# Optimization experiments

Measured on AMD Instinct MI355X. Metric: run time of the kernel, lower is better.

The kernel has to match this reference:

```python
import jax, jax.numpy as jnp
import numpy as np

RADIUS = 0.1
NSAMPLE = 32
B, N, NPOINT, C = 4, 8192, 2048, 64


def ball_query(xyz, new_xyz, fps_idx):
    """Faithful to pointnet2 ball_query CUDA kernel: for each centroid collect up to
    NSAMPLE in-radius point indices in scan order; slots beyond the count are padded
    with the first in-radius index (0 if the ball is empty). fps_idx is prepended."""
    n = xyz.shape[1]
    # squared distances (B, npoint, N)
    d2 = jnp.sum((new_xyz[:, :, None, :] - xyz[:, None, :, :]) ** 2, axis=-1)
    valid = d2 < jnp.float32(RADIUS) ** 2
    cand = jnp.where(valid, jnp.arange(n, dtype=jnp.int32), jnp.int32(n))
    cand = jnp.sort(cand, axis=-1)[:, :, :NSAMPLE]  # first NSAMPLE valid ids, N = sentinel
    first = cand[:, :, :1]
    pad = jnp.where(first < n, first, 0)            # pad with first valid (0 if none)
    idx = jnp.where(cand < n, cand, pad)
    return jnp.concatenate([fps_idx[:, :, None], idx], axis=2)  # (B, npoint, NSAMPLE+1)


def group(features, idx):
    # features (B, C, N), idx (B, npoint, K) -> (B, C, npoint, K)
    return jax.vmap(lambda f, i: f[:, i])(features, idx)


def setup_inputs() -> dict:
    key = jax.random.key(0)
    k1, k2, k3 = jax.random.split(key, 3)
    xyz = jax.random.uniform(k1, (B, N, 3), dtype=jnp.float32)
    fps_idx = jax.random.randint(k2, (B, NPOINT), 0, N, dtype=jnp.int32)
    new_xyz = jax.vmap(lambda p, i: p[i])(xyz, fps_idx)  # centroids are real points
    features = jax.random.normal(k3, (B, C, N), dtype=jnp.float32)
    return {"xyz": xyz, "new_xyz": new_xyz, "features": features, "fps_idx": fps_idx}


def reference(xyz, new_xyz, features, fps_idx):
    idx = jax.lax.stop_gradient(ball_query(xyz, new_xyz, fps_idx))
    grouped_xyz = group(jnp.swapaxes(xyz, 1, 2), idx)              # (B, 3, npoint, K)
    centered = grouped_xyz - jnp.swapaxes(new_xyz, 1, 2)[..., None]
    # NOTE: the torch module uses in-place `grouped_xyz -= ...`, so raw_grouped_xyz
    # aliases the centered tensor -> both concat slots hold centered coordinates.
    grouped_features = group(features, idx)                        # (B, C, npoint, K)
    return jnp.concatenate([centered, centered, grouped_features], axis=1)
```

## Files before the change

kernel.cpp:

```cpp
#include <hip/hip_runtime.h>
#include <stdint.h>
#include <limits.h>

constexpr int BB      = 4;
constexpr int NN      = 8192;
constexpr int NPOINT  = 2048;
constexpr int CC      = 64;
constexpr int NSAMPLE = 32;
constexpr int KTOT    = NSAMPLE + 1;
constexpr int NCH     = 3 + 3 + CC;
constexpr int CHS     = NPOINT * KTOT;

constexpr int   GG     = 5;
constexpr int   NCELL  = GG * GG * GG;
constexpr float RPADF  = 0.1001f;
constexpr int   CAND_CAP = 192;

__device__ __forceinline__ int cell_of(float x, float y, float z) {
    int ix = (int)floorf(x * 5.0f); ix = ix < 0 ? 0 : (ix > 4 ? 4 : ix);
    int iy = (int)floorf(y * 5.0f); iy = iy < 0 ? 0 : (iy > 4 ? 4 : iy);
    int iz = (int)floorf(z * 5.0f); iz = iz < 0 ? 0 : (iz > 4 ? 4 : iz);
    return (ix * GG + iy) * GG + iz;
}

__global__ __launch_bounds__(1024) void grid_hist_scan(
    const float* __restrict__ xyz, int* __restrict__ cellstartg,
    int* __restrict__ cursorg)
{
    __shared__ int hist[NCELL];
    __shared__ int csl[NCELL + 1];
    const int b = blockIdx.x;
    const int t = threadIdx.x;
    if (t < NCELL) hist[t] = 0;
    __syncthreads();
    const float* xb = xyz + (size_t)b * NN * 3;
#pragma unroll
    for (int k = 0; k < NN / 1024; ++k) {
        const float* p = xb + (size_t)(t + k * 1024) * 3;
        atomicAdd(&hist[cell_of(p[0], p[1], p[2])], 1);
    }
    __syncthreads();
    if (t < 64) {
        int x0 = hist[t];
        int x1 = (t + 64 < NCELL) ? hist[t + 64] : 0;
#pragma unroll
        for (int d = 1; d < 64; d <<= 1) {
            int t0 = __shfl_up(x0, d);
            int t1 = __shfl_up(x1, d);
            if (t >= d) { x0 += t0; x1 += t1; }
        }
        x1 += __shfl(x0, 63);
        if (t == 0) csl[0] = 0;
        csl[1 + t] = x0;
        if (t <= 60) csl[65 + t] = x1;
    }
    __syncthreads();
    if (t < NCELL + 1) cellstartg[b * (NCELL + 1) + t] = csl[t];
    if (t < NCELL)     cursorg[b * NCELL + t]          = csl[t];
}

__global__ __launch_bounds__(256) void scatter_aos(
    const float* __restrict__ xyz, int* __restrict__ cursor,
    float4* __restrict__ spt)
{
    const int t = blockIdx.x * 256 + threadIdx.x;
    if (t >= BB * NN) return;
    const int b = t >> 13;
    const int n = t & (NN - 1);
    const float* p = xyz + (size_t)t * 3;
    const float x = p[0], y = p[1], z = p[2];
    const int c = cell_of(x, y, z);
    const int pos = atomicAdd(&cursor[b * NCELL + c], 1);
    spt[b * NN + pos] = make_float4(x, y, z, __int_as_float(n));
}

__global__ __launch_bounds__(256) void ball_query_grid(
    const float4* __restrict__ spt, const int* __restrict__ cellstart,
    const float* __restrict__ new_xyz, const int* __restrict__ fps_idx,
    int*         __restrict__ idx_out)
{
    __shared__ int cand[4][CAND_CAP];
    const int w    = threadIdx.x >> 6;
    const int lane = threadIdx.x & 63;
    const int wave = blockIdx.x * 4 + w;
    const int b    = wave >> 11;

    const float* cp = new_xyz + (size_t)wave * 3;
    const float cx = cp[0], cy = cp[1], cz = cp[2];
    const float r2 = __fmul_rn(0.1f, 0.1f);

    int ix0 = (int)floorf((cx - RPADF) * 5.0f); ix0 = ix0 < 0 ? 0 : ix0;
    int ix1 = (int)floorf((cx + RPADF) * 5.0f); ix1 = ix1 > 4 ? 4 : ix1;
    int iy0 = (int)floorf((cy - RPADF) * 5.0f); iy0 = iy0 < 0 ? 0 : iy0;
    int iy1 = (int)floorf((cy + RPADF) * 5.0f); iy1 = iy1 > 4 ? 4 : iy1;
    int iz0 = (int)floorf((cz - RPADF) * 5.0f); iz0 = iz0 < 0 ? 0 : iz0;
    int iz1 = (int)floorf((cz + RPADF) * 5.0f); iz1 = iz1 > 4 ? 4 : iz1;

    const int* cs = cellstart + b * (NCELL + 1);
    const int gb  = b * NN;
    int cnt = 0;

    for (int ix = ix0; ix <= ix1; ++ix) {
        for (int iy = iy0; iy <= iy1; ++iy) {
            const int cbase = (ix * GG + iy) * GG;
            const int st = cs[cbase + iz0];
            const int en = cs[cbase + iz1 + 1];
            for (int base = st; base < en; base += 64) {
                const int pos = base + lane;
                const bool inb = pos < en;
                const float4 q = spt[gb + (inb ? pos : st)];
                const int oid = __float_as_int(q.w);
                const float dx = __fsub_rn(cx, q.x);
                const float dy = __fsub_rn(cy, q.y);
                const float dz = __fsub_rn(cz, q.z);
                const float d2 = __fadd_rn(__fadd_rn(__fmul_rn(dx, dx), __fmul_rn(dy, dy)),
                                           __fmul_rn(dz, dz));
                const bool valid = inb && (d2 < r2);
                const unsigned long long m = __ballot(valid);
                if (m != 0ull) {
                    const int prefix = __builtin_amdgcn_mbcnt_hi(
                        (unsigned)(m >> 32), __builtin_amdgcn_mbcnt_lo((unsigned)m, 0u));
                    const int slot = cnt + prefix;
                    if (valid && slot < CAND_CAP) cand[w][slot] = oid;
                    cnt += (int)__popcll(m);
                }
            }
        }
    }

    const int K = cnt > CAND_CAP ? CAND_CAP : cnt;

    int v0 = (lane       < K) ? cand[w][lane]       : INT_MAX;
    int v1 = (lane + 64  < K) ? cand[w][lane + 64]  : INT_MAX;
    int v2 = (lane + 128 < K) ? cand[w][lane + 128] : INT_MAX;
    int rk0 = 0, rk1 = 0, rk2 = 0;
    for (int j = 0; j < K; ++j) {
        const int sv = cand[w][j];
        rk0 += (sv < v0); rk1 += (sv < v1); rk2 += (sv < v2);
    }
    int* out = idx_out + (size_t)wave * KTOT;
    if (lane       < K && rk0 < NSAMPLE) out[1 + rk0] = v0;
    if (lane + 64  < K && rk1 < NSAMPLE) out[1 + rk1] = v1;
    if (lane + 128 < K && rk2 < NSAMPLE) out[1 + rk2] = v2;

    if (K < NSAMPLE) {
        int mn = v0;
#pragma unroll
        for (int off = 32; off >= 1; off >>= 1) {
            const int o = __shfl_xor(mn, off);
            mn = o < mn ? o : mn;
        }
        const int pad = (K > 0) ? mn : 0;
        if (lane >= K && lane < NSAMPLE) out[1 + lane] = pad;
    }
    if (lane == 0) out[0] = fps_idx[wave];
}

__global__ __launch_bounds__(256) void feat_transpose(
    const float* __restrict__ f, float* __restrict__ ft)
{
    __shared__ float tile[64 * 65];
    const int blk = blockIdx.x;
    const int b   = blk >> 7;
    const int n0  = (blk & 127) << 6;
    const int w   = threadIdx.x >> 6, l = threadIdx.x & 63;
#pragma unroll
    for (int i = 0; i < 16; ++i) {
        const int c = i * 4 + w;
        tile[l * 65 + c] = f[((size_t)b * CC + c) * NN + n0 + l];
    }
    __syncthreads();
#pragma unroll
    for (int i = 0; i < 16; ++i) {
        const int flat = i * 256 + threadIdx.x;
        ft[((size_t)b * NN + n0) * CC + flat] = tile[(flat >> 6) * 65 + (flat & 63)];
    }
}

__global__ __launch_bounds__(256) void gather_v4(
    const float* __restrict__ xyz, const float* __restrict__ new_xyz,
    const float4* __restrict__ ft4, const int* __restrict__ idx,
    float* __restrict__ out)
{
    const int gt = blockIdx.x * 256 + threadIdx.x;
    const int o  = gt >> 2;
    const int g  = gt & 3;
    if (o >= BB * CHS) return;
    const int id = idx[o];
    const int b  = o / CHS;
    const int jj = o - b * CHS;
    const size_t outbase = (size_t)b * NCH * CHS + jj;

    if (g < 3) {
        const float pv = xyz[(size_t)(b * NN + id) * 3 + g];
        const float cv = new_xyz[(size_t)(o / KTOT) * 3 + g];
        const float d  = __fsub_rn(pv, cv);
        out[outbase + (size_t)g * CHS]       = d;
        out[outbase + (size_t)(g + 3) * CHS] = d;
    }

    const float4* row = ft4 + ((size_t)b * NN + id) * (CC / 4);
    float4 v[4];
#pragma unroll
    for (int i = 0; i < 4; ++i) v[i] = row[i * 4 + g];
#pragma unroll
    for (int i = 0; i < 4; ++i) {
        const size_t base = outbase + (size_t)(6 + 16 * i + 4 * g) * CHS;
        out[base]           = v[i].x;
        out[base + CHS]     = v[i].y;
        out[base + 2 * CHS] = v[i].z;
        out[base + 3 * CHS] = v[i].w;
    }
}

__global__ __launch_bounds__(256) void ball_query_bf(
    const float* __restrict__ xyz, const float* __restrict__ new_xyz,
    const int* __restrict__ fps_idx, int* __restrict__ idx_out)
{
    const int wave = (blockIdx.x * blockDim.x + threadIdx.x) >> 6;
    const int lane = threadIdx.x & 63;
    if (wave >= BB * NPOINT) return;
    const int b = wave >> 11;
    const float* cp = new_xyz + (size_t)wave * 3;
    const float cx = cp[0], cy = cp[1], cz = cp[2];
    const float r2 = __fmul_rn(0.1f, 0.1f);
    const float* xb = xyz + (size_t)b * NN * 3;
    int* out = idx_out + (size_t)wave * KTOT;
    int count = 0, first = 0;
    for (int base = 0; base < NN; base += 64) {
        const int p = base + lane;
        const float dx = __fsub_rn(cx, xb[p * 3 + 0]);
        const float dy = __fsub_rn(cy, xb[p * 3 + 1]);
        const float dz = __fsub_rn(cz, xb[p * 3 + 2]);
        const float d2 = __fadd_rn(__fadd_rn(__fmul_rn(dx, dx), __fmul_rn(dy, dy)),
                                   __fmul_rn(dz, dz));
        const bool valid = d2 < r2;
        const unsigned long long m = __ballot(valid);
        if (count == 0 && m != 0ull) first = base + __builtin_ctzll(m);
        const int prefix = __builtin_amdgcn_mbcnt_hi(
            (unsigned)(m >> 32), __builtin_amdgcn_mbcnt_lo((unsigned)m, 0u));
        const int slot = count + prefix;
        if (valid && slot < NSAMPLE) out[1 + slot] = p;
        count += (int)__popcll(m);
        if (count >= NSAMPLE) break;
    }
    if (count < NSAMPLE) {
        const int pad = (count > 0) ? first : 0;
        if (lane >= count && lane < NSAMPLE) out[1 + lane] = pad;
    }
    if (lane == 0) out[0] = fps_idx[wave];
}

__global__ __launch_bounds__(256) void gather_kernel(
    const float* __restrict__ xyz, const float* __restrict__ new_xyz,
    const float* __restrict__ features, const int* __restrict__ idx,
    float* __restrict__ out)
{
    const long long total = (long long)BB * NCH * CHS;
    const long long o = (long long)blockIdx.x * blockDim.x + threadIdx.x;
    if (o >= total) return;
    const int s  = (int)(o % KTOT);
    long long t  = o / KTOT;
    const int j  = (int)(t % NPOINT);
    t /= NPOINT;
    const int ch = (int)(t % NCH);
    const int b  = (int)(t / NCH);
    const int id = idx[(long long)(b * NPOINT + j) * KTOT + s];
    float v;
    if (ch < 6) {
        const int c3 = (ch >= 3) ? (ch - 3) : ch;
        v = __fsub_rn(xyz[((long long)b * NN + id) * 3 + c3],
                      new_xyz[((long long)b * NPOINT + j) * 3 + c3]);
    } else {
        v = features[((long long)b * CC + (ch - 6)) * NN + id];
    }
    out[o] = v;
}

extern "C" void kernel_launch(void* const* d_in, const int* in_sizes, int n_in,
                              void* d_out, int out_size, void* d_ws, size_t ws_size,
                              hipStream_t stream) {
    const float* xyz      = (const float*)d_in[0];
    const float* new_xyz  = (const float*)d_in[1];
    const float* features = (const float*)d_in[2];
    const int*   fps_idx  = (const int*)d_in[3];
    float*       out      = (float*)d_out;

    const size_t off_idx  = 0;
    const size_t sz_idx   = (size_t)BB * CHS * 4;
    const size_t off_ft   = off_idx + sz_idx;
    const size_t sz_ft    = (size_t)BB * NN * CC * 4;
    const size_t off_spt  = off_ft + sz_ft;
    const size_t sz_spt   = (size_t)BB * NN * 16;
    const size_t off_cs   = off_spt + sz_spt;
    const size_t sz_cs    = (size_t)BB * (NCELL + 1) * 4;
    const size_t off_cur  = off_cs + 2048;
    const size_t need_full = off_cur + 2048;

    int* idxbuf = (int*)((char*)d_ws + off_idx);
    const int gblocks4 = (BB * CHS * 4 + 255) / 256;

    if (ws_size >= need_full) {
        float*  ft   = (float*) ((char*)d_ws + off_ft);
        float4* spt  = (float4*)((char*)d_ws + off_spt);
        int*    cs   = (int*)   ((char*)d_ws + off_cs);
        int*    cur  = (int*)   ((char*)d_ws + off_cur);

        grid_hist_scan<<<BB, 1024, 0, stream>>>(xyz, cs, cur);
        scatter_aos<<<(BB * NN) / 256, 256, 0, stream>>>(xyz, cur, spt);

        ball_query_grid<<<BB * NPOINT / 4, 256, 0, stream>>>(
            spt, cs, new_xyz, fps_idx, idxbuf);

        feat_transpose<<<BB * (NN / 64), 256, 0, stream>>>(features, ft);
        gather_v4<<<gblocks4, 256, 0, stream>>>(xyz, new_xyz, (const float4*)ft,
                                                idxbuf, out);
    } else if (ws_size >= sz_idx) {
        ball_query_bf<<<BB * NPOINT / 4, 256, 0, stream>>>(xyz, new_xyz, fps_idx, idxbuf);
        const long long total = (long long)BB * NCH * CHS;
        gather_kernel<<<(int)((total + 255) / 256), 256, 0, stream>>>(
            xyz, new_xyz, features, idxbuf, out);
    }
}
```

Measured before the change: 133.9 us.

## Fuse grid histogram with scatter and stage gather output through shared-memory tile

Merges the grid histogram/scan kernel and the scatter kernel into one per-batch kernel that keeps point coordinates and cell ids in registers and uses shared-memory cursors instead of global atomics. This removes one launch and the global cursor round-trip. The gather kernel is rewritten so each block handles 64 output positions: it fills a padded shared tile with centered xyz and feature values, then writes every channel row as fully coalesced 64-wide stores. This replaces the earlier scattered per-channel stores. The fused grid build runs on only 4 blocks, which may serialize the scatter work that previously spread across many blocks.

```diff
diff --git a/kernel.cpp b/kernel.cpp
--- a/kernel.cpp
+++ b/kernel.cpp
@@ -23,21 +23,26 @@
     return (ix * GG + iy) * GG + iz;
 }
 
-__global__ __launch_bounds__(1024) void grid_hist_scan(
+__global__ __launch_bounds__(1024) void grid_build(
     const float* __restrict__ xyz, int* __restrict__ cellstartg,
-    int* __restrict__ cursorg)
+    float4* __restrict__ spt)
 {
     __shared__ int hist[NCELL];
     __shared__ int csl[NCELL + 1];
+    __shared__ int cur[NCELL];
     const int b = blockIdx.x;
     const int t = threadIdx.x;
     if (t < NCELL) hist[t] = 0;
     __syncthreads();
     const float* xb = xyz + (size_t)b * NN * 3;
+    float px[NN / 1024], py[NN / 1024], pz[NN / 1024];
+    int   pc[NN / 1024];
 #pragma unroll
     for (int k = 0; k < NN / 1024; ++k) {
         const float* p = xb + (size_t)(t + k * 1024) * 3;
-        atomicAdd(&hist[cell_of(p[0], p[1], p[2])], 1);
+        px[k] = p[0]; py[k] = p[1]; pz[k] = p[2];
+        pc[k] = cell_of(px[k], py[k], pz[k]);
+        atomicAdd(&hist[pc[k]], 1);
     }
     __syncthreads();
     if (t < 64) {
@@ -56,22 +61,14 @@
     }
     __syncthreads();
     if (t < NCELL + 1) cellstartg[b * (NCELL + 1) + t] = csl[t];
-    if (t < NCELL)     cursorg[b * NCELL + t]          = csl[t];
-}
-
-__global__ __launch_bounds__(256) void scatter_aos(
-    const float* __restrict__ xyz, int* __restrict__ cursor,
-    float4* __restrict__ spt)
-{
-    const int t = blockIdx.x * 256 + threadIdx.x;
-    if (t >= BB * NN) return;
-    const int b = t >> 13;
-    const int n = t & (NN - 1);
-    const float* p = xyz + (size_t)t * 3;
-    const float x = p[0], y = p[1], z = p[2];
-    const int c = cell_of(x, y, z);
-    const int pos = atomicAdd(&cursor[b * NCELL + c], 1);
-    spt[b * NN + pos] = make_float4(x, y, z, __int_as_float(n));
+    if (t < NCELL)     cur[t] = csl[t];
+    __syncthreads();
+#pragma unroll
+    for (int k = 0; k < NN / 1024; ++k) {
+        const int pos = atomicAdd(&cur[pc[k]], 1);
+        spt[b * NN + pos] = make_float4(px[k], py[k], pz[k],
+                                        __int_as_float(t + k * 1024));
+    }
 }
 
 __global__ __launch_bounds__(256) void ball_query_grid(
@@ -177,39 +174,56 @@
     }
 }
 
-__global__ __launch_bounds__(256) void gather_v4(
+constexpr int TPAD = 66;
+__global__ __launch_bounds__(256) void gather_v7(
     const float* __restrict__ xyz, const float* __restrict__ new_xyz,
     const float4* __restrict__ ft4, const int* __restrict__ idx,
     float* __restrict__ out)
 {
-    const int gt = blockIdx.x * 256 + threadIdx.x;
-    const int o  = gt >> 2;
-    const int g  = gt & 3;
-    if (o >= BB * CHS) return;
-    const int id = idx[o];
-    const int b  = o / CHS;
-    const int jj = o - b * CHS;
-    const size_t outbase = (size_t)b * NCH * CHS + jj;
-
-    if (g < 3) {
-        const float pv = xyz[(size_t)(b * NN + id) * 3 + g];
-        const float cv = new_xyz[(size_t)(o / KTOT) * 3 + g];
-        const float d  = __fsub_rn(pv, cv);
-        out[outbase + (size_t)g * CHS]       = d;
-        out[outbase + (size_t)(g + 3) * CHS] = d;
-    }
-
-    const float4* row = ft4 + ((size_t)b * NN + id) * (CC / 4);
-    float4 v[4];
-#pragma unroll
-    for (int i = 0; i < 4; ++i) v[i] = row[i * 4 + g];
-#pragma unroll
-    for (int i = 0; i < 4; ++i) {
-        const size_t base = outbase + (size_t)(6 + 16 * i + 4 * g) * CHS;
-        out[base]           = v[i].x;
-        out[base + CHS]     = v[i].y;
-        out[base + 2 * CHS] = v[i].z;
-        out[base + 3 * CHS] = v[i].w;
+    __shared__ float tile[NCH][TPAD];
+    const int blk = blockIdx.x;
+    const int t   = threadIdx.x;
+    const int jj0 = blk * 64;
+    const int b   = jj0 / CHS;
+    const int jjb = jj0 - b * CHS;
+
+    if (t < 64) {
+        const int id = idx[jj0 + t];
+        const int j  = (jjb + t) / KTOT;
+        const float* gp = xyz + (size_t)(b * NN + id) * 3;
+        const float* cp = new_xyz + (size_t)(b * NPOINT + j) * 3;
+        const float vx = __fsub_rn(gp[0], cp[0]);
+        const float vy = __fsub_rn(gp[1], cp[1]);
+        const float vz = __fsub_rn(gp[2], cp[2]);
+        tile[0][t] = vx; tile[1][t] = vy; tile[2][t] = vz;
+        tile[3][t] = vx; tile[4][t] = vy; tile[5][t] = vz;
+    }
+
+    {
+        const int r = t >> 2, g = t & 3;
+        const int id = idx[jj0 + r];
+        const float4* row = ft4 + ((size_t)b * NN + id) * (CC / 4);
+        float4 v[4];
+#pragma unroll
+        for (int i = 0; i < 4; ++i) v[i] = row[4 * i + g];
+#pragma unroll
+        for (int i = 0; i < 4; ++i) {
+            const int c0 = 6 + 16 * i + 4 * g;
+            tile[c0 + 0][r] = v[i].x;
+            tile[c0 + 1][r] = v[i].y;
+            tile[c0 + 2][r] = v[i].z;
+            tile[c0 + 3][r] = v[i].w;
+        }
+    }
+    __syncthreads();
+
+    const int w   = t >> 6;
+    const int col = t & 63;
+    const size_t ob = (size_t)b * NCH * CHS + (size_t)jjb + col;
+#pragma unroll
+    for (int k = 0; k < 18; ++k) {
+        const int ch = 4 * k + w;
+        if (ch < NCH) out[ob + (size_t)ch * CHS] = tile[ch][col];
     }
 }
 
@@ -293,28 +307,23 @@
     const size_t off_spt  = off_ft + sz_ft;
     const size_t sz_spt   = (size_t)BB * NN * 16;
     const size_t off_cs   = off_spt + sz_spt;
-    const size_t sz_cs    = (size_t)BB * (NCELL + 1) * 4;
-    const size_t off_cur  = off_cs + 2048;
-    const size_t need_full = off_cur + 2048;
+    const size_t need_full = off_cs + 2048;
 
     int* idxbuf = (int*)((char*)d_ws + off_idx);
-    const int gblocks4 = (BB * CHS * 4 + 255) / 256;
 
     if (ws_size >= need_full) {
-        float*  ft   = (float*) ((char*)d_ws + off_ft);
-        float4* spt  = (float4*)((char*)d_ws + off_spt);
-        int*    cs   = (int*)   ((char*)d_ws + off_cs);
-        int*    cur  = (int*)   ((char*)d_ws + off_cur);
-
-        grid_hist_scan<<<BB, 1024, 0, stream>>>(xyz, cs, cur);
-        scatter_aos<<<(BB * NN) / 256, 256, 0, stream>>>(xyz, cur, spt);
+        float*  ft  = (float*) ((char*)d_ws + off_ft);
+        float4* spt = (float4*)((char*)d_ws + off_spt);
+        int*    cs  = (int*)   ((char*)d_ws + off_cs);
+
+        grid_build<<<BB, 1024, 0, stream>>>(xyz, cs, spt);
 
         ball_query_grid<<<BB * NPOINT / 4, 256, 0, stream>>>(
             spt, cs, new_xyz, fps_idx, idxbuf);
 
         feat_transpose<<<BB * (NN / 64), 256, 0, stream>>>(features, ft);
-        gather_v4<<<gblocks4, 256, 0, stream>>>(xyz, new_xyz, (const float4*)ft,
-                                                idxbuf, out);
+        gather_v7<<<BB * CHS / 64, 256, 0, stream>>>(xyz, new_xyz, (const float4*)ft,
+                                                     idxbuf, out);
     } else if (ws_size >= sz_idx) {
         ball_query_bf<<<BB * NPOINT / 4, 256, 0, stream>>>(xyz, new_xyz, fps_idx, idxbuf);
         const long long total = (long long)BB * NCH * CHS;
```

Measured after the change: 124.1 us. 1.08x faster.
